# Performance work log

Hardware: AMD Instinct MI355X
Metric: run time of the kernel (lower is better)

The kernel has to match this reference:

```python
import jax, jax.numpy as jnp
import numpy as np

N, IN_F, OUT_F = 8192, 512, 256
ALPHA = 0.2  # LeakyReLU negative slope
NEG_INF = -9e15


def setup_inputs() -> dict:
    key = jax.random.key(0)
    k1, k2, k3, k4 = jax.random.split(key, 4)
    input = jax.random.normal(k1, (N, IN_F), dtype=jnp.float32)
    adj = jax.random.randint(k2, (N, N), 0, 2, dtype=jnp.int32)
    # Xavier-like scale for params
    W = jax.random.normal(k3, (IN_F, OUT_F), dtype=jnp.float32) * (1.414 * np.sqrt(2.0 / (IN_F + OUT_F)))
    a = jax.random.normal(k4, (2 * OUT_F, 1), dtype=jnp.float32) * (1.414 * np.sqrt(2.0 / (2 * OUT_F + 1)))
    return {"input": input, "adj": adj, "W": W, "a": a}


def reference(input, adj, W, a):
    h = input @ W                                   # [N, F]
    a1, a2 = a[:OUT_F, 0], a[OUT_F:, 0]             # [F], [F]
    # e[i, j] = leakyrelu(h_i . a1 + h_j . a2) -- equivalent to concat+linear
    s1 = h @ a1                                     # [N]
    s2 = h @ a2                                     # [N]
    e = jax.nn.leaky_relu(s1[:, None] + s2[None, :], negative_slope=ALPHA)  # [N, N]
    e = jnp.where(adj > 0, e, NEG_INF)
    attention = jax.nn.softmax(e, axis=1)           # row-wise softmax
    # dropout p=0.0 / eval mode -> identity
    h_prime = attention @ h                          # [N, F]
    return jax.nn.elu(h_prime)                       # concat=True -> elu
```

## Files before the change

### kernel.cpp

```cpp
#include <hip/hip_runtime.h>
#include <stdint.h>

#define N_NODES 8192
#define IN_FEAT 512
#define OUT_FEAT 256
#define LOG2E 1.4426950408889634f

typedef __bf16 b16x8 __attribute__((ext_vector_type(8)));
typedef unsigned short u16x8v __attribute__((ext_vector_type(8)));
typedef float f32x4 __attribute__((ext_vector_type(4)));

static __device__ __forceinline__ unsigned short f2bf(float f) {
    union { float f; uint32_t u; } v; v.f = f;
    uint32_t r = v.u + 0x7FFFu + ((v.u >> 16) & 1u);
    return (unsigned short)(r >> 16);
}

__global__ __launch_bounds__(256) void k0_transpose_w(const float* __restrict__ W,
                                                      unsigned short* __restrict__ Wt) {
    int tid = blockIdx.x * 256 + threadIdx.x;
    int c = tid & (OUT_FEAT - 1);
    int k = tid >> 8;
    Wt[(size_t)c * IN_FEAT + k] = f2bf(W[(size_t)k * OUT_FEAT + c]);
}

__global__ __launch_bounds__(256) void k1_hgemm(const float* __restrict__ input,
                                                const unsigned short* __restrict__ Wt,
                                                const float* __restrict__ a_vec,
                                                unsigned short* __restrict__ hTf,
                                                float* __restrict__ s1_raw,
                                                float* __restrict__ s2_raw) {
    int tid = threadIdx.x;
    int lane = tid & 63;
    int c = lane & 15, g = lane >> 4;
    int r0 = blockIdx.x * 64 + (tid >> 6) * 16;
    f32x4 acc[16];
#pragma unroll
    for (int t = 0; t < 16; ++t) acc[t] = (f32x4){0.f, 0.f, 0.f, 0.f};
    const float* arow = input + (size_t)(r0 + c) * IN_FEAT;
#pragma unroll 1
    for (int kk = 0; kk < IN_FEAT / 32; ++kk) {
        int kb = kk * 32 + 8 * g;
        float4 x0 = *(const float4*)(arow + kb);
        float4 x1 = *(const float4*)(arow + kb + 4);
        u16x8v au;
        au[0] = f2bf(x0.x); au[1] = f2bf(x0.y); au[2] = f2bf(x0.z); au[3] = f2bf(x0.w);
        au[4] = f2bf(x1.x); au[5] = f2bf(x1.y); au[6] = f2bf(x1.z); au[7] = f2bf(x1.w);
        b16x8 af = __builtin_bit_cast(b16x8, au);
#pragma unroll
        for (int t = 0; t < 16; ++t) {
            b16x8 bf = __builtin_bit_cast(b16x8,
                *(const u16x8v*)(Wt + (size_t)(16 * t + c) * IN_FEAT + kb));
            acc[t] = __builtin_amdgcn_mfma_f32_16x16x32_bf16(af, bf, acc[t], 0, 0, 0);
        }
    }
    float a1v[16], a2v[16];
#pragma unroll
    for (int t = 0; t < 16; ++t) {
        a1v[t] = a_vec[16 * t + c];
        a2v[t] = a_vec[OUT_FEAT + 16 * t + c];
    }
#pragma unroll
    for (int r = 0; r < 4; ++r) {
        float s1p = 0.f, s2p = 0.f;
#pragma unroll
        for (int t = 0; t < 16; ++t) { s1p += acc[t][r] * a1v[t]; s2p += acc[t][r] * a2v[t]; }
#pragma unroll
        for (int m = 1; m <= 8; m <<= 1) { s1p += __shfl_xor(s1p, m); s2p += __shfl_xor(s2p, m); }
        if (c == 0) {
            int row = r0 + 4 * g + r;
            s1_raw[row] = s1p;
            s2_raw[row] = s2p;
        }
    }
    int chunk = r0 >> 5;
    int lp = ((r0 & 16) >> 3) + (g >> 1);
    int e0 = 4 * (g & 1);
#pragma unroll
    for (int t = 0; t < 16; ++t) {
        ushort4 pk;
        pk.x = f2bf(acc[t][0]); pk.y = f2bf(acc[t][1]);
        pk.z = f2bf(acc[t][2]); pk.w = f2bf(acc[t][3]);
        *(ushort4*)(hTf + ((size_t)(chunk * 16 + t) * 64 + lp * 16 + c) * 8 + e0) = pk;
    }
}

__global__ __launch_bounds__(256) void k2_prep(const float* __restrict__ s1_raw,
                                               const float* __restrict__ s2_raw,
                                               float* __restrict__ s2k,
                                               float2* __restrict__ row2) {
    __shared__ float red[256];
    int tid = threadIdx.x;
    float m = -3.0e38f;
    for (int j = tid; j < N_NODES; j += 256) m = fmaxf(m, s2_raw[j]);
    red[tid] = m;
    __syncthreads();
    for (int s = 128; s > 0; s >>= 1) {
        if (tid < s) red[tid] = fmaxf(red[tid], red[tid + s]);
        __syncthreads();
    }
    float M2 = red[0];
    int i = blockIdx.x * 256 + tid;
    float s1 = s1_raw[i];
    float u = s1 + M2;
    float mi = fmaxf(u, 0.2f * u);
    row2[i] = make_float2((s1 - mi) * LOG2E, -0.8f * mi * LOG2E);
    s2k[i] = s2_raw[i] * LOG2E;
}

__global__ __launch_bounds__(256, 2) void k3_flash(const int* __restrict__ adj,
                                                   const unsigned short* __restrict__ hTf,
                                                   const float* __restrict__ s2k,
                                                   const float2* __restrict__ row2,
                                                   float* __restrict__ pout,
                                                   float* __restrict__ rowpart) {
    __shared__ __align__(16) unsigned short tiles[2][8192];
    __shared__ uint32_t lmaskD[2][64];
    __shared__ __align__(16) float ls2k[2048];

    int tid = threadIdx.x;
    int w = tid >> 6, lane = tid & 63;
    int c = lane & 15, g = lane >> 4;
    int ch = w & 1, rq = w >> 1;
    int jq = blockIdx.x & 3;
    int rg = blockIdx.x >> 2;
    int rowbase = rg * 64 + rq * 32;

    int mrow = tid >> 2;
    int mg8 = tid & 3;
    const int* adjbase = adj + (size_t)(rg * 64 + mrow) * N_NODES + jq * 2048 + mg8 * 8;

    *(float4*)&ls2k[tid * 8]     = *(const float4*)(s2k + jq * 2048 + tid * 8);
    *(float4*)&ls2k[tid * 8 + 4] = *(const float4*)(s2k + jq * 2048 + tid * 8 + 4);
    {
        int jc = jq * 64;
#pragma unroll
        for (int q = 0; q < 4; ++q) {
            int ti = w * 4 + q;
            const unsigned short* src = hTf + (size_t)jc * 8192 + (size_t)(ti * 64 + lane) * 8;
            __builtin_amdgcn_global_load_lds(
                (const __attribute__((address_space(1))) uint32_t*)src,
                (__attribute__((address_space(3))) uint32_t*)(&tiles[0][ti * 512]), 16, 0, 0);
        }
    }
    {
        int4 v0 = *(const int4*)(adjbase);
        int4 v1 = *(const int4*)(adjbase + 4);
        unsigned b = (unsigned)(v0.x != 0) | ((unsigned)(v0.y != 0) << 1)
                   | ((unsigned)(v0.z != 0) << 2) | ((unsigned)(v0.w != 0) << 3)
                   | ((unsigned)(v1.x != 0) << 4) | ((unsigned)(v1.y != 0) << 5)
                   | ((unsigned)(v1.z != 0) << 6) | ((unsigned)(v1.w != 0) << 7);
        ((unsigned char*)&lmaskD[0][mrow])[mg8] = (unsigned char)b;
    }

    float2 rc0 = row2[rowbase + c];
    float2 rc1 = row2[rowbase + 16 + c];
    float a_row0 = rc0.x, m8_0 = rc0.y;
    float a_row1 = rc1.x, m8_1 = rc1.y;

    f32x4 acc0[8], acc1[8];
#pragma unroll
    for (int t = 0; t < 8; ++t) { acc0[t] = (f32x4){0,0,0,0}; acc1[t] = (f32x4){0,0,0,0}; }
    float lacc0 = 0.f, lacc1 = 0.f;

#pragma unroll 2
    for (int kk = 0; kk < 64; ++kk) {
        int cur = kk & 1;
        __syncthreads();

        int4 v0, v1;
        bool have_next = (kk < 63);
        if (have_next) {
            int jc = jq * 64 + kk + 1;
#pragma unroll
            for (int q = 0; q < 4; ++q) {
                int ti = w * 4 + q;
                const unsigned short* src = hTf + (size_t)jc * 8192 + (size_t)(ti * 64 + lane) * 8;
                __builtin_amdgcn_global_load_lds(
                    (const __attribute__((address_space(1))) uint32_t*)src,
                    (__attribute__((address_space(3))) uint32_t*)(&tiles[cur ^ 1][ti * 512]), 16, 0, 0);
            }
            v0 = *(const int4*)(adjbase + (kk + 1) * 32);
            v1 = *(const int4*)(adjbase + (kk + 1) * 32 + 4);
        }

        uint32_t md0 = lmaskD[cur][rq * 32 + c];
        uint32_t md1 = lmaskD[cur][rq * 32 + 16 + c];
        uint32_t mb0 = (md0 >> (8 * g)) & 0xFFu;
        uint32_t mb1 = (md1 >> (8 * g)) & 0xFFu;
        const float* sp = &ls2k[kk * 32 + 8 * g];
        float4 s0 = *(const float4*)sp;
        float4 s1v = *(const float4*)(sp + 4);
        float sv[8] = {s0.x, s0.y, s0.z, s0.w, s1v.x, s1v.y, s1v.z, s1v.w};
        b16x8 af0, af1;
#pragma unroll
        for (int e = 0; e < 8; ++e) {
            float va = a_row0 + sv[e];
            float vb = __builtin_fmaf(va, 0.2f, m8_0);
            float p0 = (mb0 & (1u << e)) ? __builtin_amdgcn_exp2f(fmaxf(va, vb)) : 0.f;
            lacc0 += p0;
            af0[e] = (__bf16)p0;
            float vc = a_row1 + sv[e];
            float vd = __builtin_fmaf(vc, 0.2f, m8_1);
            float p1 = (mb1 & (1u << e)) ? __builtin_amdgcn_exp2f(fmaxf(vc, vd)) : 0.f;
            lacc1 += p1;
            af1[e] = (__bf16)p1;
        }

        const unsigned short* tb = &tiles[cur][ch * 8 * 512];
#pragma unroll
        for (int t = 0; t < 8; ++t) {
            b16x8 bf = __builtin_bit_cast(b16x8, *(const u16x8v*)(tb + t * 512 + lane * 8));
            acc0[t] = __builtin_amdgcn_mfma_f32_16x16x32_bf16(af0, bf, acc0[t], 0, 0, 0);
            acc1[t] = __builtin_amdgcn_mfma_f32_16x16x32_bf16(af1, bf, acc1[t], 0, 0, 0);
        }

        if (have_next) {
            unsigned b = (unsigned)(v0.x != 0) | ((unsigned)(v0.y != 0) << 1)
                       | ((unsigned)(v0.z != 0) << 2) | ((unsigned)(v0.w != 0) << 3)
                       | ((unsigned)(v1.x != 0) << 4) | ((unsigned)(v1.y != 0) << 5)
                       | ((unsigned)(v1.z != 0) << 6) | ((unsigned)(v1.w != 0) << 7);
            ((unsigned char*)&lmaskD[cur ^ 1][mrow])[mg8] = (unsigned char)b;
        }
    }

    float l0 = lacc0 + __shfl_xor(lacc0, 16); l0 += __shfl_xor(l0, 32);
    float l1 = lacc1 + __shfl_xor(lacc1, 16); l1 += __shfl_xor(l1, 32);
    if (ch == 0 && g == 0) {
        rowpart[jq * N_NODES + rowbase + c] = l0;
        rowpart[jq * N_NODES + rowbase + 16 + c] = l1;
    }

#pragma unroll
    for (int r = 0; r < 4; ++r) {
        int grow0 = rowbase + 4 * g + r;
        int grow1 = grow0 + 16;
#pragma unroll
        for (int t = 0; t < 8; ++t) {
            pout[((size_t)jq * N_NODES + grow0) * OUT_FEAT + ch * 128 + 16 * t + c] = acc0[t][r];
            pout[((size_t)jq * N_NODES + grow1) * OUT_FEAT + ch * 128 + 16 * t + c] = acc1[t][r];
        }
    }
}

__global__ __launch_bounds__(256) void k4_reduce(const float* __restrict__ pout,
                                                 const float* __restrict__ rowpart,
                                                 float* __restrict__ out) {
    int t = blockIdx.x * 256 + threadIdx.x;
    int row = t >> 8;
    float s = 0.f, l = 0.f;
#pragma unroll
    for (int q = 0; q < 4; ++q) {
        s += pout[(size_t)q * N_NODES * OUT_FEAT + t];
        l += rowpart[q * N_NODES + row];
    }
    float inv = (l > 0.f) ? 1.0f / l : 0.f;
    float x = s * inv;
    out[t] = (x > 0.f) ? x : (__builtin_amdgcn_exp2f(x * LOG2E) - 1.0f);
}

extern "C" void kernel_launch(void* const* d_in, const int* in_sizes, int n_in,
                              void* d_out, int out_size, void* d_ws, size_t ws_size,
                              hipStream_t stream) {
    const float* input = (const float*)d_in[0];
    const int* adj = (const int*)d_in[1];
    const float* W = (const float*)d_in[2];
    const float* a_vec = (const float*)d_in[3];
    float* out = (float*)d_out;

    char* ws = (char*)d_ws;
    unsigned short* Wt  = (unsigned short*)(ws);
    unsigned short* hTf = (unsigned short*)(ws + 262144);
    float*  s2k     = (float*)(ws + 4456448);
    float2* row2    = (float2*)(ws + 4489216);
    float*  s1_raw  = (float*)(ws + 4554752);
    float*  s2_raw  = (float*)(ws + 4587520);
    float*  rowpart = (float*)(ws + 13008896);
    float*  pout    = (float*)(ws + 13139968);

    hipLaunchKernelGGL(k0_transpose_w, dim3(512), dim3(256), 0, stream, W, Wt);
    hipLaunchKernelGGL(k1_hgemm, dim3(N_NODES / 64), dim3(256), 0, stream,
                       input, Wt, a_vec, hTf, s1_raw, s2_raw);
    hipLaunchKernelGGL(k2_prep, dim3(32), dim3(256), 0, stream, s1_raw, s2_raw, s2k, row2);
    hipLaunchKernelGGL(k3_flash, dim3(512), dim3(256), 0, stream,
                       adj, hTf, s2k, row2, pout, rowpart);
    hipLaunchKernelGGL(k4_reduce, dim3(N_NODES * OUT_FEAT / 256), dim3(256), 0, stream,
                       pout, rowpart, out);
}
```

Measured before the change: 177.6 us.

## Factor exp out of attention loop, prepack adjacency bits, read hT directly

Rewrites the flash kernel's score computation as a product of precomputed per-row and per-column exponentials, using exp(leaky(x)) = max(e^x, e^{0.2x}). This removes the per-element exp2 from the inner loop. Adjacency is packed to a bitmask in a separate pass, and the LDS double-buffered tile staging and barriers are dropped in favour of direct global reads of hT and mask words. The trade-offs are possible fp32 overflow or underflow in the factored exponentials, an extra pass over adj, and loss of LDS reuse and prefetch for the hT tiles.

```diff
diff --git a/kernel.cpp b/kernel.cpp
--- a/kernel.cpp
+++ b/kernel.cpp
@@ -14,6 +14,23 @@
     union { float f; uint32_t u; } v; v.f = f;
     uint32_t r = v.u + 0x7FFFu + ((v.u >> 16) & 1u);
     return (unsigned short)(r >> 16);
+}
+
+__global__ __launch_bounds__(256) void k_pack(const int* __restrict__ adj,
+                                              unsigned char* __restrict__ bitsR) {
+    size_t t = (size_t)blockIdx.x * 256 + threadIdx.x;
+    const int4* a4 = (const int4*)adj + t * 2;
+    int4 x0 = a4[0];
+    int4 x1 = a4[1];
+    unsigned b = (unsigned)(x0.x != 0)
+               | ((unsigned)(x0.y != 0) << 1)
+               | ((unsigned)(x0.z != 0) << 2)
+               | ((unsigned)(x0.w != 0) << 3)
+               | ((unsigned)(x1.x != 0) << 4)
+               | ((unsigned)(x1.y != 0) << 5)
+               | ((unsigned)(x1.z != 0) << 6)
+               | ((unsigned)(x1.w != 0) << 7);
+    bitsR[t] = (unsigned char)b;
 }
 
 __global__ __launch_bounds__(256) void k0_transpose_w(const float* __restrict__ W,
@@ -87,7 +104,7 @@
 
 __global__ __launch_bounds__(256) void k2_prep(const float* __restrict__ s1_raw,
                                                const float* __restrict__ s2_raw,
-                                               float* __restrict__ s2k,
+                                               float* __restrict__ e12,
                                                float2* __restrict__ row2) {
     __shared__ float red[256];
     int tid = threadIdx.x;
@@ -104,19 +121,20 @@
     float s1 = s1_raw[i];
     float u = s1 + M2;
     float mi = fmaxf(u, 0.2f * u);
-    row2[i] = make_float2((s1 - mi) * LOG2E, -0.8f * mi * LOG2E);
-    s2k[i] = s2_raw[i] * LOG2E;
-}
-
-__global__ __launch_bounds__(256, 2) void k3_flash(const int* __restrict__ adj,
+    row2[i] = make_float2(__builtin_amdgcn_exp2f((s1 - mi) * LOG2E),
+                          __builtin_amdgcn_exp2f((0.2f * s1 - mi) * LOG2E));
+    float s2 = s2_raw[i];
+    e12[2 * i]     = __builtin_amdgcn_exp2f(s2 * LOG2E);
+    e12[2 * i + 1] = __builtin_amdgcn_exp2f(0.2f * s2 * LOG2E);
+}
+
+__global__ __launch_bounds__(256, 2) void k3_flash(const uint32_t* __restrict__ maskR,
                                                    const unsigned short* __restrict__ hTf,
-                                                   const float* __restrict__ s2k,
+                                                   const float* __restrict__ e12g,
                                                    const float2* __restrict__ row2,
                                                    float* __restrict__ pout,
                                                    float* __restrict__ rowpart) {
-    __shared__ __align__(16) unsigned short tiles[2][8192];
-    __shared__ uint32_t lmaskD[2][64];
-    __shared__ __align__(16) float ls2k[2048];
+    __shared__ __align__(16) float le12[4096];
 
     int tid = threadIdx.x;
     int w = tid >> 6, lane = tid & 63;
@@ -126,37 +144,19 @@
     int rg = blockIdx.x >> 2;
     int rowbase = rg * 64 + rq * 32;
 
-    int mrow = tid >> 2;
-    int mg8 = tid & 3;
-    const int* adjbase = adj + (size_t)(rg * 64 + mrow) * N_NODES + jq * 2048 + mg8 * 8;
-
-    *(float4*)&ls2k[tid * 8]     = *(const float4*)(s2k + jq * 2048 + tid * 8);
-    *(float4*)&ls2k[tid * 8 + 4] = *(const float4*)(s2k + jq * 2048 + tid * 8 + 4);
-    {
-        int jc = jq * 64;
-#pragma unroll
-        for (int q = 0; q < 4; ++q) {
-            int ti = w * 4 + q;
-            const unsigned short* src = hTf + (size_t)jc * 8192 + (size_t)(ti * 64 + lane) * 8;
-            __builtin_amdgcn_global_load_lds(
-                (const __attribute__((address_space(1))) uint32_t*)src,
-                (__attribute__((address_space(3))) uint32_t*)(&tiles[0][ti * 512]), 16, 0, 0);
-        }
-    }
-    {
-        int4 v0 = *(const int4*)(adjbase);
-        int4 v1 = *(const int4*)(adjbase + 4);
-        unsigned b = (unsigned)(v0.x != 0) | ((unsigned)(v0.y != 0) << 1)
-                   | ((unsigned)(v0.z != 0) << 2) | ((unsigned)(v0.w != 0) << 3)
-                   | ((unsigned)(v1.x != 0) << 4) | ((unsigned)(v1.y != 0) << 5)
-                   | ((unsigned)(v1.z != 0) << 6) | ((unsigned)(v1.w != 0) << 7);
-        ((unsigned char*)&lmaskD[0][mrow])[mg8] = (unsigned char)b;
-    }
-
+#pragma unroll
+    for (int q = 0; q < 4; ++q) {
+        *(float4*)&le12[tid * 16 + q * 4] =
+            *(const float4*)(e12g + (size_t)jq * 4096 + tid * 16 + q * 4);
+    }
     float2 rc0 = row2[rowbase + c];
     float2 rc1 = row2[rowbase + 16 + c];
-    float a_row0 = rc0.x, m8_0 = rc0.y;
-    float a_row1 = rc1.x, m8_1 = rc1.y;
+    float E1r0 = rc0.x, E2r0 = rc0.y;
+    float E1r1 = rc1.x, E2r1 = rc1.y;
+    __syncthreads();
+
+    const int4* m4_0 = (const int4*)maskR + (size_t)(rowbase + c) * 64 + jq * 16;
+    const int4* m4_1 = (const int4*)maskR + (size_t)(rowbase + 16 + c) * 64 + jq * 16;
 
     f32x4 acc0[8], acc1[8];
 #pragma unroll
@@ -164,63 +164,41 @@
     float lacc0 = 0.f, lacc1 = 0.f;
 
 #pragma unroll 2
-    for (int kk = 0; kk < 64; ++kk) {
-        int cur = kk & 1;
-        __syncthreads();
-
-        int4 v0, v1;
-        bool have_next = (kk < 63);
-        if (have_next) {
-            int jc = jq * 64 + kk + 1;
-#pragma unroll
-            for (int q = 0; q < 4; ++q) {
-                int ti = w * 4 + q;
-                const unsigned short* src = hTf + (size_t)jc * 8192 + (size_t)(ti * 64 + lane) * 8;
-                __builtin_amdgcn_global_load_lds(
-                    (const __attribute__((address_space(1))) uint32_t*)src,
-                    (__attribute__((address_space(3))) uint32_t*)(&tiles[cur ^ 1][ti * 512]), 16, 0, 0);
+    for (int kk4 = 0; kk4 < 16; ++kk4) {
+        int4 mq0 = m4_0[kk4];
+        int4 mq1 = m4_1[kk4];
+        uint32_t md0[4] = {(uint32_t)mq0.x, (uint32_t)mq0.y, (uint32_t)mq0.z, (uint32_t)mq0.w};
+        uint32_t md1[4] = {(uint32_t)mq1.x, (uint32_t)mq1.y, (uint32_t)mq1.z, (uint32_t)mq1.w};
+#pragma unroll
+        for (int sub = 0; sub < 4; ++sub) {
+            int kk = kk4 * 4 + sub;
+            int jchunk = jq * 64 + kk;
+            uint32_t mb0 = (md0[sub] >> (8 * g)) & 0xFFu;
+            uint32_t mb1 = (md1[sub] >> (8 * g)) & 0xFFu;
+            float ev[16];
+#pragma unroll
+            for (int q = 0; q < 4; ++q)
+                *(f32x4*)&ev[q * 4] = *(const f32x4*)&le12[(kk * 32 + 8 * g) * 2 + q * 4];
+            b16x8 af0, af1;
+#pragma unroll
+            for (int e = 0; e < 8; ++e) {
+                float e1 = ev[2 * e], e2 = ev[2 * e + 1];
+                float q0 = fmaxf(E1r0 * e1, E2r0 * e2);
+                float p0 = (mb0 & (1u << e)) ? q0 : 0.f;
+                lacc0 += p0;
+                af0[e] = (__bf16)p0;
+                float q1 = fmaxf(E1r1 * e1, E2r1 * e2);
+                float p1 = (mb1 & (1u << e)) ? q1 : 0.f;
+                lacc1 += p1;
+                af1[e] = (__bf16)p1;
             }
-            v0 = *(const int4*)(adjbase + (kk + 1) * 32);
-            v1 = *(const int4*)(adjbase + (kk + 1) * 32 + 4);
-        }
-
-        uint32_t md0 = lmaskD[cur][rq * 32 + c];
-        uint32_t md1 = lmaskD[cur][rq * 32 + 16 + c];
-        uint32_t mb0 = (md0 >> (8 * g)) & 0xFFu;
-        uint32_t mb1 = (md1 >> (8 * g)) & 0xFFu;
-        const float* sp = &ls2k[kk * 32 + 8 * g];
-        float4 s0 = *(const float4*)sp;
-        float4 s1v = *(const float4*)(sp + 4);
-        float sv[8] = {s0.x, s0.y, s0.z, s0.w, s1v.x, s1v.y, s1v.z, s1v.w};
-        b16x8 af0, af1;
-#pragma unroll
-        for (int e = 0; e < 8; ++e) {
-            float va = a_row0 + sv[e];
-            float vb = __builtin_fmaf(va, 0.2f, m8_0);
-            float p0 = (mb0 & (1u << e)) ? __builtin_amdgcn_exp2f(fmaxf(va, vb)) : 0.f;
-            lacc0 += p0;
-            af0[e] = (__bf16)p0;
-            float vc = a_row1 + sv[e];
-            float vd = __builtin_fmaf(vc, 0.2f, m8_1);
-            float p1 = (mb1 & (1u << e)) ? __builtin_amdgcn_exp2f(fmaxf(vc, vd)) : 0.f;
-            lacc1 += p1;
-            af1[e] = (__bf16)p1;
-        }
-
-        const unsigned short* tb = &tiles[cur][ch * 8 * 512];
-#pragma unroll
-        for (int t = 0; t < 8; ++t) {
-            b16x8 bf = __builtin_bit_cast(b16x8, *(const u16x8v*)(tb + t * 512 + lane * 8));
-            acc0[t] = __builtin_amdgcn_mfma_f32_16x16x32_bf16(af0, bf, acc0[t], 0, 0, 0);
-            acc1[t] = __builtin_amdgcn_mfma_f32_16x16x32_bf16(af1, bf, acc1[t], 0, 0, 0);
-        }
-
-        if (have_next) {
-            unsigned b = (unsigned)(v0.x != 0) | ((unsigned)(v0.y != 0) << 1)
-                       | ((unsigned)(v0.z != 0) << 2) | ((unsigned)(v0.w != 0) << 3)
-                       | ((unsigned)(v1.x != 0) << 4) | ((unsigned)(v1.y != 0) << 5)
-                       | ((unsigned)(v1.z != 0) << 6) | ((unsigned)(v1.w != 0) << 7);
-            ((unsigned char*)&lmaskD[cur ^ 1][mrow])[mg8] = (unsigned char)b;
+            const unsigned short* tb = hTf + (size_t)(jchunk * 16 + ch * 8) * 512 + lane * 8;
+#pragma unroll
+            for (int t = 0; t < 8; ++t) {
+                b16x8 bf = __builtin_bit_cast(b16x8, *(const u16x8v*)(tb + t * 512));
+                acc0[t] = __builtin_amdgcn_mfma_f32_16x16x32_bf16(af0, bf, acc0[t], 0, 0, 0);
+                acc1[t] = __builtin_amdgcn_mfma_f32_16x16x32_bf16(af1, bf, acc1[t], 0, 0, 0);
+            }
         }
     }
 
@@ -271,19 +249,21 @@
     char* ws = (char*)d_ws;
     unsigned short* Wt  = (unsigned short*)(ws);
     unsigned short* hTf = (unsigned short*)(ws + 262144);
-    float*  s2k     = (float*)(ws + 4456448);
-    float2* row2    = (float2*)(ws + 4489216);
-    float*  s1_raw  = (float*)(ws + 4554752);
-    float*  s2_raw  = (float*)(ws + 4587520);
-    float*  rowpart = (float*)(ws + 13008896);
-    float*  pout    = (float*)(ws + 13139968);
-
+    float*  e12     = (float*)(ws + 4456448);
+    float2* row2    = (float2*)(ws + 4521984);
+    float*  s1_raw  = (float*)(ws + 4587520);
+    float*  s2_raw  = (float*)(ws + 4620288);
+    unsigned char* bitsR = (unsigned char*)(ws + 4653056);
+    float*  rowpart = (float*)(ws + 13041664);
+    float*  pout    = (float*)(ws + 13172736);
+
+    hipLaunchKernelGGL(k_pack, dim3(32768), dim3(256), 0, stream, adj, bitsR);
     hipLaunchKernelGGL(k0_transpose_w, dim3(512), dim3(256), 0, stream, W, Wt);
     hipLaunchKernelGGL(k1_hgemm, dim3(N_NODES / 64), dim3(256), 0, stream,
                        input, Wt, a_vec, hTf, s1_raw, s2_raw);
-    hipLaunchKernelGGL(k2_prep, dim3(32), dim3(256), 0, stream, s1_raw, s2_raw, s2k, row2);
+    hipLaunchKernelGGL(k2_prep, dim3(32), dim3(256), 0, stream, s1_raw, s2_raw, e12, row2);
     hipLaunchKernelGGL(k3_flash, dim3(512), dim3(256), 0, stream,
-                       adj, hTf, s2k, row2, pout, rowpart);
+                       (const uint32_t*)bitsR, hTf, e12, row2, pout, rowpart);
     hipLaunchKernelGGL(k4_reduce, dim3(N_NODES * OUT_FEAT / 256), dim3(256), 0, stream,
                        pout, rowpart, out);
 }
```

After: 260.5 us. +46.6%, slower.
